# Performance work log

Hardware: AMD Instinct MI355X
Metric: run time of the kernel (lower is better)

The kernel has to match this reference:

```python
import jax, jax.numpy as jnp
from jax import lax
import numpy as np

S, B, D, H, F, K = 1024, 8, 512, 8, 2048, 31
HD = D // H
EPS = 1e-5


def _ln(x, g, b):
    m = jnp.mean(x, axis=-1, keepdims=True)
    v = jnp.mean((x - m) ** 2, axis=-1, keepdims=True)
    return (x - m) * lax.rsqrt(v + EPS) * g + b


def _swish(x):
    return x * jax.nn.sigmoid(x)


def setup_inputs() -> dict:
    key = jax.random.key(0)
    ks = iter(jax.random.split(key, 64))

    def rn(shape, scale=0.02):
        return jax.random.normal(next(ks), shape, dtype=jnp.float32) * scale

    inp = {
        'src': jax.random.normal(next(ks), (S, B, D), dtype=jnp.float32),
        'pos_emb': jax.random.normal(next(ks), (1, 2 * S - 1, D), dtype=jnp.float32),
        # macaron FFN
        'ffm_w1': rn((F, D)), 'ffm_b1': jnp.zeros((F,), jnp.float32),
        'ffm_w2': rn((D, F)), 'ffm_b2': jnp.zeros((D,), jnp.float32),
        # rel-pos MHA
        'in_w': rn((3 * D, D)), 'in_b': jnp.zeros((3 * D,), jnp.float32),
        'out_w': rn((D, D)), 'out_b': jnp.zeros((D,), jnp.float32),
        'pos_w': rn((D, D)),
        'bias_u': rn((H, HD), 0.1), 'bias_v': rn((H, HD), 0.1),
        # conv module
        'pw1_w': rn((2 * D, D)), 'pw1_b': jnp.zeros((2 * D,), jnp.float32),
        'dw_w': rn((D, 1, K)), 'dw_b': jnp.zeros((D,), jnp.float32),
        'cnorm_g': jnp.ones((D,), jnp.float32), 'cnorm_b': jnp.zeros((D,), jnp.float32),
        'pw2_w': rn((D, D)), 'pw2_b': jnp.zeros((D,), jnp.float32),
        # final FFN
        'ff_w1': rn((F, D)), 'ff_b1': jnp.zeros((F,), jnp.float32),
        'ff_w2': rn((D, F)), 'ff_b2': jnp.zeros((D,), jnp.float32),
        # layer norms
        'g_ffm': jnp.ones((D,), jnp.float32), 'b_ffm': jnp.zeros((D,), jnp.float32),
        'g_mha': jnp.ones((D,), jnp.float32), 'b_mha': jnp.zeros((D,), jnp.float32),
        'g_conv': jnp.ones((D,), jnp.float32), 'b_conv': jnp.zeros((D,), jnp.float32),
        'g_ff': jnp.ones((D,), jnp.float32), 'b_ff': jnp.zeros((D,), jnp.float32),
        'g_fin': jnp.ones((D,), jnp.float32), 'b_fin': jnp.zeros((D,), jnp.float32),
    }
    return inp


def _ffn(x, w1, b1, w2, b2):
    return _swish(x @ w1.T + b1) @ w2.T + b2


def _attn(x, pos_emb, in_w, in_b, out_w, out_b, pos_w, bias_u, bias_v):
    # x: (S, B, D)
    qkv = x @ in_w.T + in_b  # (S, B, 3D)
    q, k, v = jnp.split(qkv, 3, axis=-1)
    q = q.reshape(S, B, H, HD).transpose(1, 2, 0, 3)  # (B, H, S, HD)
    k = k.reshape(S, B, H, HD).transpose(1, 2, 0, 3)
    v = v.reshape(S, B, H, HD).transpose(1, 2, 0, 3)
    # positional projection: (2S-1, D) -> (H, HD, 2S-1)
    p = (pos_emb[0] @ pos_w.T).reshape(2 * S - 1, H, HD).transpose(1, 2, 0)
    ac = jnp.einsum('bhsd,bhtd->bhst', q + bias_u[None, :, None, :], k)
    bd = jnp.einsum('bhsd,hdn->bhsn', q + bias_v[None, :, None, :], p)
    # rel_shift: out[b,h,i,j] = bd[b,h,i, (S-1) - i + j]
    idx = (S - 1) - jnp.arange(S)[:, None] + jnp.arange(S)[None, :]  # (S, S)
    bd = jnp.take_along_axis(bd, idx[None, None], axis=-1)  # (B, H, S, S)
    w = jax.nn.softmax((ac + bd) * (HD ** -0.5), axis=-1)
    o = jnp.einsum('bhst,bhtd->bhsd', w, v)
    o = o.transpose(2, 0, 1, 3).reshape(S, B, D)
    return o @ out_w.T + out_b


def _conv_module(x, pw1_w, pw1_b, dw_w, dw_b, cnorm_g, cnorm_b, pw2_w, pw2_b):
    # x: (S, B, D) -> (B, 2D, S)
    y = jnp.einsum('sbd,ed->bes', x, pw1_w) + pw1_b[None, :, None]
    a, g = jnp.split(y, 2, axis=1)
    y = a * jax.nn.sigmoid(g)  # GLU over channels, (B, D, S)
    pad = (K - 1) // 2
    y = lax.conv_general_dilated(y, dw_w, (1,), [(pad, pad)],
                                 dimension_numbers=('NCH', 'OIH', 'NCH'),
                                 feature_group_count=D) + dw_b[None, :, None]
    y = _ln(y.transpose(0, 2, 1), cnorm_g, cnorm_b)  # (B, S, D)
    y = _swish(y)
    y = y @ pw2_w.T + pw2_b  # pointwise conv2 == per-position linear
    return y.transpose(1, 0, 2)  # (S, B, D)


def reference(src, pos_emb, ffm_w1, ffm_b1, ffm_w2, ffm_b2, in_w, in_b, out_w,
              out_b, pos_w, bias_u, bias_v, pw1_w, pw1_b, dw_w, dw_b, cnorm_g,
              cnorm_b, pw2_w, pw2_b, ff_w1, ff_b1, ff_w2, ff_b2, g_ffm, b_ffm,
              g_mha, b_mha, g_conv, b_conv, g_ff, b_ff, g_fin, b_fin):
    x = src
    x = x + 0.5 * _ffn(_ln(x, g_ffm, b_ffm), ffm_w1, ffm_b1, ffm_w2, ffm_b2)
    x = x + _attn(_ln(x, g_mha, b_mha), pos_emb, in_w, in_b, out_w, out_b,
                  pos_w, bias_u, bias_v)
    x = x + _conv_module(_ln(x, g_conv, b_conv), pw1_w, pw1_b, dw_w, dw_b,
                         cnorm_g, cnorm_b, pw2_w, pw2_b)
    x = x + _ffn(_ln(x, g_ff, b_ff), ff_w1, ff_b1, ff_w2, ff_b2)
    return _ln(x, g_fin, b_fin)
```

## Files before the change

### kernel.cpp

```cpp
#include <hip/hip_runtime.h>

typedef __attribute__((ext_vector_type(8))) short bf16x8;
typedef __attribute__((ext_vector_type(4))) short s16x4;
typedef __attribute__((ext_vector_type(4))) float f32x4;
typedef unsigned int u32;

#define SQ 1024
#define BB 8
#define DM 512
#define NH 8
#define HD 64
#define FF 2048
#define NROWS (SQ*BB)

static __device__ __forceinline__ float b2f(short s) {
  return __uint_as_float(((u32)(unsigned short)s) << 16);
}
static __device__ __forceinline__ short f2b(float f) {
  u32 u = __float_as_uint(f);
  return (short)((u + 0x7FFFu + ((u >> 16) & 1u)) >> 16);
}
static __device__ __forceinline__ short f2bt(float f) {
  return (short)((__float_as_uint(f) + 0x8000u) >> 16);
}
static __device__ __forceinline__ float sigm(float x) { return 1.f / (1.f + __expf(-x)); }

static __device__ __forceinline__ f32x4 mfma16(bf16x8 a, bf16x8 b, f32x4 c) {
  return __builtin_amdgcn_mfma_f32_16x16x32_bf16(a, b, c, 0, 0, 0);
}

static __device__ __forceinline__ void gload16(const void* g, void* l) {
  __builtin_amdgcn_global_load_lds(
      (const __attribute__((address_space(1))) void*)g,
      (__attribute__((address_space(3))) void*)l, 16, 0, 0);
}

static __device__ __forceinline__ int swzp(int r, int byteoff) {
  return (r * 128 + byteoff) ^ ((r & 7) << 4);
}

#define WAIT_LGKM() do { \
    asm volatile("s_waitcnt lgkmcnt(0)" ::: "memory"); \
    __builtin_amdgcn_sched_barrier(0); } while (0)
#define WAIT_VM(n) do { \
    asm volatile("s_waitcnt vmcnt(" #n ")" ::: "memory"); \
    __builtin_amdgcn_sched_barrier(0); } while (0)

struct CvtArgs {
  const float* s[10];
  short* d[10];
  int n4[10];
  int cum[10];
};
__global__ __launch_bounds__(256) void cvt_multi(CvtArgs a) {
  int bid = blockIdx.x;
  int seg = 0;
#pragma unroll
  for (int i = 1; i < 10; ++i) if (bid >= a.cum[i]) seg = i;
  int idx = (bid - a.cum[seg]) * 256 + threadIdx.x;
  if (idx >= a.n4[seg]) return;
  float4 v = ((const float4*)a.s[seg])[idx];
  s16x4 r = { f2b(v.x), f2b(v.y), f2b(v.z), f2b(v.w) };
  ((s16x4*)a.d[seg])[idx] = r;
}

template<int MODE, int INF32>
__global__ __launch_bounds__(256) void ln_kernel(const void* __restrict__ xin,
                                                 const float* __restrict__ gam,
                                                 const float* __restrict__ bet,
                                                 void* __restrict__ out) {
  int w = threadIdx.x >> 6, lane = threadIdx.x & 63;
  int row = (blockIdx.x << 2) + w;
  float v[8];
  if (INF32) {
    const float* xr = (const float*)xin + (size_t)row * DM + lane * 8;
    float4 a = *(const float4*)xr;
    float4 c = *(const float4*)(xr + 4);
    v[0]=a.x; v[1]=a.y; v[2]=a.z; v[3]=a.w; v[4]=c.x; v[5]=c.y; v[6]=c.z; v[7]=c.w;
  } else {
    bf16x8 x8 = *(const bf16x8*)((const short*)xin + (size_t)row * DM + lane * 8);
#pragma unroll
    for (int e = 0; e < 8; ++e) v[e] = b2f(x8[e]);
  }
  float s = 0.f, q = 0.f;
#pragma unroll
  for (int e = 0; e < 8; ++e) { s += v[e]; q += v[e] * v[e]; }
#pragma unroll
  for (int m = 1; m < 64; m <<= 1) { s += __shfl_xor(s, m); q += __shfl_xor(q, m); }
  float mean = s * (1.f / DM);
  float rstd = rsqrtf(q * (1.f / DM) - mean * mean + 1e-5f);
  int col = lane * 8;
  if (MODE == 1) {
    float* o = (float*)out + (size_t)row * DM + col;
    float y[8];
#pragma unroll
    for (int e = 0; e < 8; ++e) y[e] = (v[e] - mean) * rstd * gam[col + e] + bet[col + e];
    *(float4*)o = make_float4(y[0], y[1], y[2], y[3]);
    *(float4*)(o + 4) = make_float4(y[4], y[5], y[6], y[7]);
  } else {
    bf16x8 r;
#pragma unroll
    for (int e = 0; e < 8; ++e) {
      float y = (v[e] - mean) * rstd * gam[col + e] + bet[col + e];
      r[e] = f2b(y);
    }
    *(bf16x8*)((short*)out + (size_t)row * DM + col) = r;
  }
}

template<int EPI>
__global__ __launch_bounds__(512, 2) void gemm256(const short* __restrict__ A,
                                                  const short* __restrict__ W,
                                                  const float* __restrict__ bias,
                                                  short* __restrict__ out,
                                                  int M, int N, int K) {
  __shared__ __align__(16) short lds[3 * 16384];
  int nb = N >> 8;
  int nwg = gridDim.x, bid = blockIdx.x;
  int bid2 = ((nwg & 7) == 0) ? ((bid & 7) * (nwg >> 3) + (bid >> 3)) : bid;
  int bm = bid2 / nb, bn = bid2 % nb;
  int m0 = bm << 8, n0 = bn << 8;
  int tid = threadIdx.x, w = tid >> 6, lane = tid & 63;
  int wm = w >> 2, wn = w & 3;
  int l15 = lane & 15, l4 = lane >> 4;
  int srow = lane >> 2;
  int slog = (lane & 3) ^ (((lane >> 5) & 1) << 1);
  int scol = slog << 3;

  const short* gsrc = (w < 4) ? (A + (size_t)(m0 + w * 64 + srow) * K + scol)
                              : (W + (size_t)(n0 + (w - 4) * 64 + srow) * K + scol);

  f32x4 acc[8][4];
#pragma unroll
  for (int i = 0; i < 8; ++i)
#pragma unroll
    for (int j = 0; j < 4; ++j) acc[i][j] = (f32x4){0.f, 0.f, 0.f, 0.f};

  auto stage2 = [&](int u, int kt, int q0) {
#pragma unroll
    for (int q = q0; q < q0 + 2; ++q)
      gload16(gsrc + (size_t)(q * 16) * K + kt,
              (char*)lds + u * 32768 + (w * 4 + q) * 1024);
  };
  auto rdA = [&](int u, int mf) -> bf16x8 {
    int ps = l4 ^ (((l15 >> 3) & 1) << 1);
    return *(const bf16x8*)((char*)lds + u * 32768 + (wm * 8 + mf) * 1024 + l15 * 64 + ps * 16);
  };
  auto rdB = [&](int u, int nf) -> bf16x8 {
    int ps = l4 ^ (((l15 >> 3) & 1) << 1);
    return *(const bf16x8*)((char*)lds + u * 32768 + 16384 + (wn * 4 + nf) * 1024 + l15 * 64 + ps * 16);
  };

  int nt = K >> 5;
  stage2(0, 0, 0); stage2(0, 0, 2);
  stage2(1, 32, 0); stage2(1, 32, 2);
  WAIT_VM(4);
  __builtin_amdgcn_s_barrier();

  int u = 0;
  for (int t = 0; t < nt; ++t) {
    int kt2 = (t + 2) << 5;
    int us = u + 2; if (us >= 3) us -= 3;
    bool st = (t + 2) < nt;
    bf16x8 afrag[4], bfrag[4];
#pragma unroll
    for (int nf = 0; nf < 4; ++nf) bfrag[nf] = rdB(u, nf);
#pragma unroll
    for (int mf = 0; mf < 4; ++mf) afrag[mf] = rdA(u, mf);
    if (st) stage2(us, kt2, 0);
    __builtin_amdgcn_s_barrier();
    WAIT_LGKM();
    __builtin_amdgcn_s_setprio(1);
#pragma unroll
    for (int mf = 0; mf < 4; ++mf)
#pragma unroll
      for (int nf = 0; nf < 4; ++nf)
        acc[mf][nf] = mfma16(afrag[mf], bfrag[nf], acc[mf][nf]);
    __builtin_amdgcn_s_setprio(0);
    __builtin_amdgcn_s_barrier();
#pragma unroll
    for (int mf = 0; mf < 4; ++mf) afrag[mf] = rdA(u, mf + 4);
    if (st) stage2(us, kt2, 2);
    __builtin_amdgcn_s_barrier();
    WAIT_LGKM();
    __builtin_amdgcn_s_setprio(1);
#pragma unroll
    for (int mf = 0; mf < 4; ++mf)
#pragma unroll
      for (int nf = 0; nf < 4; ++nf)
        acc[mf + 4][nf] = mfma16(afrag[mf], bfrag[nf], acc[mf + 4][nf]);
    __builtin_amdgcn_s_setprio(0);
    if (t < nt - 1) {
      if (st) { WAIT_VM(4); } else { WAIT_VM(0); }
    }
    __builtin_amdgcn_s_barrier();
    ++u; if (u >= 3) u -= 3;
  }

#pragma unroll
  for (int nf = 0; nf < 4; ++nf) {
    int col = n0 + wn * 64 + nf * 16 + l15;
    float bv = bias[col];
#pragma unroll
    for (int mf = 0; mf < 8; ++mf) {
#pragma unroll
      for (int r4 = 0; r4 < 4; ++r4) {
        int row = m0 + wm * 128 + mf * 16 + l4 * 4 + r4;
        float v = acc[mf][nf][r4] + bv;
        if (EPI == 1) v = v * sigm(v);
        out[(size_t)row * N + col] = f2b(v);
      }
    }
  }
}

template<int EPI, int RESF32>
__global__ __launch_bounds__(256, 3) void gemm128(const short* __restrict__ A,
                                                  const short* __restrict__ W,
                                                  const float* __restrict__ bias,
                                                  const void* __restrict__ res,
                                                  float alpha, short* __restrict__ out,
                                                  int M, int N, int K) {
  __shared__ __align__(16) short lds[3 * 8192];
  int nb = N >> 7;
  int nwg = gridDim.x, bid = blockIdx.x;
  int bid2 = ((nwg & 7) == 0) ? ((bid & 7) * (nwg >> 3) + (bid >> 3)) : bid;
  int bm = bid2 / nb, bn = bid2 % nb;
  int m0 = bm << 7, n0 = bn << 7;
  int tid = threadIdx.x, w = tid >> 6, lane = tid & 63;
  int wm = w >> 1, wn = w & 1;
  int l15 = lane & 15, l4 = lane >> 4;
  int srow = lane >> 2;
  int slog = (lane & 3) ^ (((lane >> 5) & 1) << 1);
  int scol = slog << 3;

  const short* gsrc = (w < 2) ? (A + (size_t)(m0 + w * 64 + srow) * K + scol)
                              : (W + (size_t)(n0 + (w - 2) * 64 + srow) * K + scol);
  int ldsbase = w * 4096;

  f32x4 acc[4][4];
#pragma unroll
  for (int i = 0; i < 4; ++i)
#pragma unroll
    for (int j = 0; j < 4; ++j) acc[i][j] = (f32x4){0.f, 0.f, 0.f, 0.f};

  auto stage = [&](int u, int kt) {
#pragma unroll
    for (int q = 0; q < 4; ++q)
      gload16(gsrc + (size_t)(q * 16) * K + kt,
              (char*)lds + u * 16384 + ldsbase + q * 1024);
  };
  auto rdA = [&](int u, int mf) -> bf16x8 {
    int ps = l4 ^ (((l15 >> 3) & 1) << 1);
    return *(const bf16x8*)((char*)lds + u * 16384 + (wm * 4 + mf) * 1024 + l15 * 64 + ps * 16);
  };
  auto rdB = [&](int u, int nf) -> bf16x8 {
    int ps = l4 ^ (((l15 >> 3) & 1) << 1);
    return *(const bf16x8*)((char*)lds + u * 16384 + 8192 + (wn * 4 + nf) * 1024 + l15 * 64 + ps * 16);
  };

  int nt = K >> 5;
  stage(0, 0);
  stage(1, 32);
  WAIT_VM(4);
  __builtin_amdgcn_s_barrier();

  int u = 0;
  for (int t = 0; t < nt; ++t) {
    int us = u + 2; if (us >= 3) us -= 3;
    bool st = (t + 2) < nt;
    bf16x8 afrag[4], bfrag[4];
#pragma unroll
    for (int mf = 0; mf < 4; ++mf) afrag[mf] = rdA(u, mf);
#pragma unroll
    for (int nf = 0; nf < 4; ++nf) bfrag[nf] = rdB(u, nf);
    if (st) stage(us, (t + 2) << 5);
    WAIT_LGKM();
    __builtin_amdgcn_s_setprio(1);
#pragma unroll
    for (int mf = 0; mf < 4; ++mf)
#pragma unroll
      for (int nf = 0; nf < 4; ++nf)
        acc[mf][nf] = mfma16(afrag[mf], bfrag[nf], acc[mf][nf]);
    __builtin_amdgcn_s_setprio(0);
    if (t < nt - 1) {
      if (st) { WAIT_VM(4); } else { WAIT_VM(0); }
    }
    __builtin_amdgcn_s_barrier();
    ++u; if (u >= 3) u -= 3;
  }

#pragma unroll
  for (int mf = 0; mf < 4; ++mf) {
#pragma unroll
    for (int nf = 0; nf < 4; ++nf) {
      int col = n0 + wn * 64 + nf * 16 + l15;
      float bv = (EPI == 3) ? 0.f : bias[col];
#pragma unroll
      for (int r4 = 0; r4 < 4; ++r4) {
        int row = m0 + wm * 64 + mf * 16 + l4 * 4 + r4;
        size_t idx = (size_t)row * N + col;
        float v = acc[mf][nf][r4] + bv;
        if (EPI == 0 || EPI == 3) {
          out[idx] = f2b(v);
        } else if (EPI == 1) {
          out[idx] = f2b(v * sigm(v));
        } else {
          float rv = RESF32 ? ((const float*)res)[idx] : b2f(((const short*)res)[idx]);
          out[idx] = f2b(rv + alpha * v);
        }
      }
    }
  }
}

__global__ __launch_bounds__(256) void prep_kernel(const short* __restrict__ qkv,
                                                   short* __restrict__ VTp) {
  __shared__ short ldsv[64 * 66];
  int tid = threadIdx.x;
  int st = blockIdx.x & 15, bh = blockIdx.x >> 4;
  int b = bh >> 3, h = bh & 7;
  int s0 = st << 6;
#pragma unroll
  for (int pass = 0; pass < 2; ++pass) {
    int r = pass * 32 + (tid >> 3), c = tid & 7;
    int s = s0 + r;
    bf16x8 v8 = *(const bf16x8*)(qkv + (size_t)(s * BB + b) * 1536 + 1024 + h * 64 + c * 8);
    *(bf16x8*)(ldsv + r * 66 + c * 8) = v8;
  }
  __syncthreads();
#pragma unroll
  for (int pass = 0; pass < 2; ++pass) {
    int d = pass * 32 + (tid >> 3), sc = tid & 7;
    bf16x8 o;
#pragma unroll
    for (int u = 0; u < 8; ++u) o[u] = ldsv[(sc * 8 + u) * 66 + d];
    *(bf16x8*)(VTp + ((size_t)bh * 64 + d) * SQ + s0 + sc * 8) = o;
  }
}

__global__ __launch_bounds__(512, 4) void attn_kernel(const short* __restrict__ qkv,
                                                      const short* __restrict__ VTp,
                                                      const short* __restrict__ posb,
                                                      const float* __restrict__ bias_u,
                                                      const float* __restrict__ bias_v,
                                                      short* __restrict__ obuf) {
  __shared__ __align__(16) char smem[78848];
  char* lds_k   = smem;
  char* lds_vt  = smem + 16384;
  char* lds_pos = smem + 24576;
  char* lds_ew  = smem + 57344;

  int tid = threadIdx.x, w = tid >> 6, lane = tid & 63;
  int l15 = lane & 15, l4 = lane >> 4;
  int it = blockIdx.x >> 6, bh = blockIdx.x & 63;
  int b = bh >> 3, h = bh & 7;
  int i0 = it << 7;
  char* ewb = lds_ew + w * 2688;

  const size_t hoffB = (size_t)bh * SQ * 128;

  const float SC2 = 0.125f * 1.44269504f;
  int fr = i0 + w * 16 + l15;
  const short* qrow = qkv + (size_t)(fr * BB + b) * 1536 + h * 64;
  bf16x8 qu_f[2], qv_f[2];
#pragma unroll
  for (int ks = 0; ks < 2; ++ks) {
    bf16x8 qraw = *(const bf16x8*)(qrow + ks * 32 + l4 * 8);
#pragma unroll
    for (int e = 0; e < 8; ++e) {
      float qf = b2f(qraw[e]);
      int d = h * 64 + ks * 32 + l4 * 8 + e;
      qu_f[ks][e] = f2b((qf + bias_u[d]) * SC2);
      qv_f[ks][e] = f2b((qf + bias_v[d]) * SC2);
    }
  }

  float m_run = -1e30f, l_run = 0.f;
  f32x4 o_acc[4];
#pragma unroll
  for (int dt = 0; dt < 4; ++dt) o_acc[dt] = (f32x4){0.f, 0.f, 0.f, 0.f};

  int prbase = 112 - 16 * w;
  int lnq = lane >> 3, lnr = lane & 7;
  int r8 = w * 8 + lnq;
  int byt = (lnr * 16) ^ ((r8 & 7) << 4);
  int nbase = 896 - i0;

  auto stageK = [&](int t1) {
    int j = (t1 << 6) + r8;
    gload16((const char*)qkv + (size_t)(j * BB + b) * 3072 + 1024 + h * 128 + byt,
            lds_k + (t1 & 1) * 8192 + w * 1024);
  };
  auto stageVT = [&](int t1) {
    gload16((const char*)VTp + hoffB + (size_t)r8 * 2048 + (size_t)(t1 << 7) + byt,
            lds_vt + w * 1024);
  };
  auto stagePosSeg = [&](int gbase, int pseg) {
    gload16((const char*)posb + (size_t)(gbase + r8) * 1024 + h * 128 + byt,
            lds_pos + pseg * 8192 + w * 1024);
  };

  stagePosSeg(nbase, 0);
  stagePosSeg(nbase + 64, 1);
  stagePosSeg(nbase + 128, 2);
  stageK(0);
  WAIT_VM(0);

  for (int t = 0; t < 16; ++t) {
    int cur = t & 1;
    __builtin_amdgcn_s_barrier();
    stageVT(t);

    f32x4 acs[4];
    __builtin_amdgcn_s_setprio(1);
#pragma unroll
    for (int kt = 0; kt < 4; ++kt) {
      f32x4 z = (f32x4){0.f, 0.f, 0.f, 0.f};
      bf16x8 kb0 = *(const bf16x8*)(lds_k + cur * 8192 + swzp(kt * 16 + l15, l4 * 16));
      bf16x8 kb1 = *(const bf16x8*)(lds_k + cur * 8192 + swzp(kt * 16 + l15, 64 + l4 * 16));
      z = mfma16(kb0, qu_f[0], z);
      z = mfma16(kb1, qu_f[1], z);
      acs[kt] = z;
    }
    __builtin_amdgcn_s_setprio(0);
#pragma unroll
    for (int pt = 0; pt < 5; ++pt) {
      f32x4 z = (f32x4){0.f, 0.f, 0.f, 0.f};
      int pr = prbase + pt * 16 + l15;
      char* pbase = lds_pos + (((t + (pr >> 6)) & 3) * 8192);
      bf16x8 pb0 = *(const bf16x8*)(pbase + swzp(pr & 63, l4 * 16));
      bf16x8 pb1 = *(const bf16x8*)(pbase + swzp(pr & 63, 64 + l4 * 16));
      __builtin_amdgcn_s_setprio(1);
      z = mfma16(pb0, qv_f[0], z);
      z = mfma16(pb1, qv_f[1], z);
      __builtin_amdgcn_s_setprio(0);
      s16x4 ek;
#pragma unroll
      for (int r = 0; r < 4; ++r) ek[r] = f2bt(z[r]);
      *(s16x4*)(ewb + (l15 * 84 + pt * 16 + l4 * 4) * 2) = ek;
    }

    bool pf = (t + 1) < 16;
    if (pf) {
      stageK(t + 1);
      stagePosSeg(nbase + (t << 6) + 192, (t + 3) & 3);
    }

    WAIT_LGKM();

    float sv[4][4];
#pragma unroll
    for (int kt = 0; kt < 4; ++kt) {
#pragma unroll
      for (int r = 0; r < 4; ++r) {
        int n = 15 - l15 + kt * 16 + l4 * 4 + r;
        float ev = b2f(*(const short*)(ewb + (l15 * 84 + n) * 2));
        sv[kt][r] = acs[kt][r] + ev;
      }
    }
    float mk[4];
#pragma unroll
    for (int kt = 0; kt < 4; ++kt)
      mk[kt] = fmaxf(fmaxf(sv[kt][0], sv[kt][1]), fmaxf(sv[kt][2], sv[kt][3]));
    float mt = fmaxf(fmaxf(mk[0], mk[1]), fmaxf(mk[2], mk[3]));

    if (!__all(mt <= m_run + 11.5415604f)) {
      float mr = fmaxf(mt, __shfl_xor(mt, 16));
      mr = fmaxf(mr, __shfl_xor(mr, 32));
      float mn = fmaxf(m_run, mr);
      float fac = exp2f(m_run - mn);
      m_run = mn;
      l_run *= fac;
      float fb[4];
#pragma unroll
      for (int r4 = 0; r4 < 4; ++r4) fb[r4] = __shfl(fac, (l4 << 2) + r4);
#pragma unroll
      for (int dt = 0; dt < 4; ++dt)
#pragma unroll
        for (int r4 = 0; r4 < 4; ++r4) o_acc[dt][r4] *= fb[r4];
    }
    float lsk[4];
#pragma unroll
    for (int kt = 0; kt < 4; ++kt) {
      s16x4 pk;
      float p[4];
#pragma unroll
      for (int r = 0; r < 4; ++r) {
        p[r] = exp2f(sv[kt][r] - m_run);
        pk[r] = f2bt(p[r]);
      }
      lsk[kt] = (p[0] + p[1]) + (p[2] + p[3]);
      *(s16x4*)(ewb + l15 * 128 + ((kt * 32 + l4 * 8) ^ ((l15 & 7) << 4))) = pk;
    }
    l_run += (lsk[0] + lsk[1]) + (lsk[2] + lsk[3]);

    if (pf) { WAIT_VM(2); } else { WAIT_VM(0); }
    WAIT_LGKM();
    __builtin_amdgcn_s_barrier();

    bf16x8 pa[2];
#pragma unroll
    for (int ks = 0; ks < 2; ++ks)
      pa[ks] = *(const bf16x8*)(ewb + swzp(l15, ks * 64 + l4 * 16));
    __builtin_amdgcn_s_setprio(1);
#pragma unroll
    for (int dt = 0; dt < 4; ++dt) {
      bf16x8 vb0 = *(const bf16x8*)(lds_vt + swzp(dt * 16 + l15, l4 * 16));
      bf16x8 vb1 = *(const bf16x8*)(lds_vt + swzp(dt * 16 + l15, 64 + l4 * 16));
      o_acc[dt] = mfma16(pa[0], vb0, o_acc[dt]);
      o_acc[dt] = mfma16(pa[1], vb1, o_acc[dt]);
    }
    __builtin_amdgcn_s_setprio(0);

    WAIT_VM(0);
  }

  float lt = l_run + __shfl_xor(l_run, 16);
  lt += __shfl_xor(lt, 32);
  float lb[4];
#pragma unroll
  for (int r4 = 0; r4 < 4; ++r4) lb[r4] = __shfl(lt, (l4 << 2) + r4);
#pragma unroll
  for (int dt = 0; dt < 4; ++dt) {
#pragma unroll
    for (int r4 = 0; r4 < 4; ++r4) {
      int i = i0 + w * 16 + l4 * 4 + r4;
      int d = dt * 16 + l15;
      float val = o_acc[dt][r4] / lb[r4];
      obuf[(size_t)(i * BB + b) * DM + h * 64 + d] = f2b(val);
    }
  }
}

__global__ __launch_bounds__(256) void glu_dwconv_kernel(const short* __restrict__ pw1,
                                                         const float* __restrict__ dww,
                                                         const float* __restrict__ dwb,
                                                         const float* __restrict__ cg,
                                                         const float* __restrict__ cb,
                                                         short* __restrict__ outbf) {
  __shared__ short glu[38 * 512];
  __shared__ float red[8][4][2];
  int tid = threadIdx.x;
  int b = blockIdx.x & 7;
  int s0 = (blockIdx.x >> 3) << 3;
  for (int idx = tid; idx < 38 * 64; idx += 256) {
    int r = idx >> 6, c8 = idx & 63;
    int s = s0 - 15 + r;
    bf16x8 res;
    if (s >= 0 && s < SQ) {
      const short* row = pw1 + (size_t)(s * BB + b) * 1024;
      bf16x8 a8 = *(const bf16x8*)(row + c8 * 8);
      bf16x8 g8 = *(const bf16x8*)(row + 512 + c8 * 8);
#pragma unroll
      for (int e = 0; e < 8; ++e) res[e] = f2b(b2f(a8[e]) * sigm(b2f(g8[e])));
    } else {
#pragma unroll
      for (int e = 0; e < 8; ++e) res[e] = 0;
    }
    *(bf16x8*)(glu + r * 512 + c8 * 8) = res;
  }
  __syncthreads();

  float a0[8], a1[8];
  {
    float wreg[31];
#pragma unroll
    for (int k = 0; k < 31; ++k) wreg[k] = dww[tid * 31 + k];
    float bb = dwb[tid];
    for (int ri = 0; ri < 8; ++ri) {
      float acc = bb;
#pragma unroll
      for (int k = 0; k < 31; ++k)
        acc += wreg[k] * b2f(glu[(ri + k) * 512 + tid]);
      a0[ri] = acc;
    }
  }
  {
    int d = tid + 256;
    float wreg[31];
#pragma unroll
    for (int k = 0; k < 31; ++k) wreg[k] = dww[d * 31 + k];
    float bb = dwb[d];
    for (int ri = 0; ri < 8; ++ri) {
      float acc = bb;
#pragma unroll
      for (int k = 0; k < 31; ++k)
        acc += wreg[k] * b2f(glu[(ri + k) * 512 + d]);
      a1[ri] = acc;
    }
  }

  int w = tid >> 6, lane = tid & 63;
#pragma unroll
  for (int ri = 0; ri < 8; ++ri) {
    float sp = a0[ri] + a1[ri];
    float qp = a0[ri] * a0[ri] + a1[ri] * a1[ri];
#pragma unroll
    for (int m = 1; m < 64; m <<= 1) { sp += __shfl_xor(sp, m); qp += __shfl_xor(qp, m); }
    if (lane == 0) { red[ri][w][0] = sp; red[ri][w][1] = qp; }
  }
  __syncthreads();
  float g0 = cg[tid], b0 = cb[tid], g1 = cg[tid + 256], b1 = cb[tid + 256];
#pragma unroll
  for (int ri = 0; ri < 8; ++ri) {
    float s = red[ri][0][0] + red[ri][1][0] + red[ri][2][0] + red[ri][3][0];
    float q = red[ri][0][1] + red[ri][1][1] + red[ri][2][1] + red[ri][3][1];
    float mean = s * (1.f / DM);
    float rstd = rsqrtf(q * (1.f / DM) - mean * mean + 1e-5f);
    float y0 = (a0[ri] - mean) * rstd * g0 + b0;
    float y1 = (a1[ri] - mean) * rstd * g1 + b1;
    y0 = y0 * sigm(y0);
    y1 = y1 * sigm(y1);
    size_t base = (size_t)((s0 + ri) * BB + b) * 512;
    outbf[base + tid] = f2b(y0);
    outbf[base + tid + 256] = f2b(y1);
  }
}

extern "C" void kernel_launch(void* const* d_in, const int* in_sizes, int n_in,
                              void* d_out, int out_size, void* d_ws, size_t ws_size,
                              hipStream_t stream) {
  const float* src    = (const float*)d_in[0];
  const float* pose   = (const float*)d_in[1];
  const float* ffm_w1 = (const float*)d_in[2];
  const float* ffm_b1 = (const float*)d_in[3];
  const float* ffm_w2 = (const float*)d_in[4];
  const float* ffm_b2 = (const float*)d_in[5];
  const float* in_w   = (const float*)d_in[6];
  const float* in_b   = (const float*)d_in[7];
  const float* out_w  = (const float*)d_in[8];
  const float* out_b  = (const float*)d_in[9];
  const float* pos_w  = (const float*)d_in[10];
  const float* bias_u = (const float*)d_in[11];
  const float* bias_v = (const float*)d_in[12];
  const float* pw1_w  = (const float*)d_in[13];
  const float* pw1_b  = (const float*)d_in[14];
  const float* dw_w   = (const float*)d_in[15];
  const float* dw_b   = (const float*)d_in[16];
  const float* cng    = (const float*)d_in[17];
  const float* cnb    = (const float*)d_in[18];
  const float* pw2_w  = (const float*)d_in[19];
  const float* pw2_b  = (const float*)d_in[20];
  const float* ff_w1  = (const float*)d_in[21];
  const float* ff_b1  = (const float*)d_in[22];
  const float* ff_w2  = (const float*)d_in[23];
  const float* ff_b2  = (const float*)d_in[24];
  const float* g_ffm  = (const float*)d_in[25];
  const float* b_ffm  = (const float*)d_in[26];
  const float* g_mha  = (const float*)d_in[27];
  const float* b_mha  = (const float*)d_in[28];
  const float* g_conv = (const float*)d_in[29];
  const float* b_conv = (const float*)d_in[30];
  const float* g_ff   = (const float*)d_in[31];
  const float* b_ff   = (const float*)d_in[32];
  const float* g_fin  = (const float*)d_in[33];
  const float* b_fin  = (const float*)d_in[34];

  char* ws = (char*)d_ws;
  size_t off = 0;
  auto alloc = [&](size_t bytes) -> void* {
    void* p = ws + off;
    off += (bytes + 255) & ~(size_t)255;
    return p;
  };
  short* wb_ffm1 = (short*)alloc((size_t)FF * DM * 2);
  short* wb_ffm2 = (short*)alloc((size_t)DM * FF * 2);
  short* wb_in   = (short*)alloc((size_t)3 * DM * DM * 2);
  short* wb_out  = (short*)alloc((size_t)DM * DM * 2);
  short* wb_pos  = (short*)alloc((size_t)DM * DM * 2);
  short* wb_pw1  = (short*)alloc((size_t)2 * DM * DM * 2);
  short* wb_pw2  = (short*)alloc((size_t)DM * DM * 2);
  short* wb_ff1  = (short*)alloc((size_t)FF * DM * 2);
  short* wb_ff2  = (short*)alloc((size_t)DM * FF * 2);
  short* pos_src = (short*)alloc((size_t)2048 * DM * 2);
  short* pos_bf  = (short*)alloc((size_t)2048 * DM * 2);
  short* lnb     = (short*)alloc((size_t)NROWS * DM * 2);
  short* hbig    = (short*)alloc((size_t)NROWS * FF * 2);
  short* qkvb    = (short*)alloc((size_t)NROWS * 3 * DM * 2);
  short* obuf    = (short*)alloc((size_t)NROWS * DM * 2);
  short* x1      = (short*)alloc((size_t)NROWS * DM * 2);
  short* x2      = (short*)alloc((size_t)NROWS * DM * 2);
  short* pw1raw  = hbig;
  short* convy   = obuf;
  short* x3 = x1;
  short* x4 = x2;
  short* VTp = hbig + (size_t)3 * 4194304;

  CvtArgs ca;
  const float* srcs[10] = {ffm_w1, ffm_w2, in_w, out_w, pos_w, pw1_w, pw2_w, ff_w1, ff_w2, pose};
  short* dsts[10] = {wb_ffm1, wb_ffm2, wb_in, wb_out, wb_pos, wb_pw1, wb_pw2, wb_ff1, wb_ff2, pos_src};
  size_t ns[10] = {(size_t)FF*DM, (size_t)DM*FF, (size_t)3*DM*DM, (size_t)DM*DM, (size_t)DM*DM,
                   (size_t)2*DM*DM, (size_t)DM*DM, (size_t)FF*DM, (size_t)DM*FF, (size_t)2047*DM};
  int cum = 0;
  for (int i = 0; i < 10; ++i) {
    ca.s[i] = srcs[i]; ca.d[i] = dsts[i];
    ca.n4[i] = (int)(ns[i] >> 2);
    ca.cum[i] = cum;
    cum += (ca.n4[i] + 255) / 256;
  }
  cvt_multi<<<dim3(cum), dim3(256), 0, stream>>>(ca);

  auto gemmR = [&](int RESF32, const short* A, const short* W, const float* bias,
                   const void* res, float alpha, short* out, int M, int N, int K) {
    dim3 g((M / 128) * (N / 128)), blk(256);
    if (RESF32) gemm128<2, 1><<<g, blk, 0, stream>>>(A, W, bias, res, alpha, out, M, N, K);
    else        gemm128<2, 0><<<g, blk, 0, stream>>>(A, W, bias, res, alpha, out, M, N, K);
  };
  auto gemm2 = [&](int EPI, const short* A, const short* W, const float* bias,
                   short* out, int M, int N, int K) {
    dim3 g((M / 256) * (N / 256)), blk(512);
    if (EPI == 0) gemm256<0><<<g, blk, 0, stream>>>(A, W, bias, out, M, N, K);
    else          gemm256<1><<<g, blk, 0, stream>>>(A, W, bias, out, M, N, K);
  };

  gemm128<3, 0><<<dim3((2048 / 128) * (512 / 128)), dim3(256), 0, stream>>>(
      pos_src, wb_pos, nullptr, nullptr, 0.f, pos_bf, 2048, DM, DM);

  ln_kernel<0, 1><<<dim3(NROWS / 4), dim3(256), 0, stream>>>(src, g_ffm, b_ffm, lnb);
  gemm2(1, lnb, wb_ffm1, ffm_b1, hbig, NROWS, FF, DM);
  gemmR(1, hbig, wb_ffm2, ffm_b2, src, 0.5f, x1, NROWS, DM, FF);

  ln_kernel<0, 0><<<dim3(NROWS / 4), dim3(256), 0, stream>>>(x1, g_mha, b_mha, lnb);
  gemm128<0, 0><<<dim3((NROWS / 128) * (3 * DM / 128)), dim3(256), 0, stream>>>(
      lnb, wb_in, in_b, nullptr, 0.f, qkvb, NROWS, 3 * DM, DM);
  prep_kernel<<<dim3(1024), dim3(256), 0, stream>>>(qkvb, VTp);
  attn_kernel<<<dim3(512), dim3(512), 0, stream>>>(qkvb, VTp, pos_bf, bias_u, bias_v, obuf);
  gemmR(0, obuf, wb_out, out_b, x1, 1.f, x2, NROWS, DM, DM);

  ln_kernel<0, 0><<<dim3(NROWS / 4), dim3(256), 0, stream>>>(x2, g_conv, b_conv, lnb);
  gemm128<0, 0><<<dim3((NROWS / 128) * (2 * DM / 128)), dim3(256), 0, stream>>>(
      lnb, wb_pw1, pw1_b, nullptr, 0.f, pw1raw, NROWS, 2 * DM, DM);
  glu_dwconv_kernel<<<dim3(1024), dim3(256), 0, stream>>>(pw1raw, dw_w, dw_b, cng, cnb, convy);
  gemmR(0, convy, wb_pw2, pw2_b, x2, 1.f, x3, NROWS, DM, DM);

  ln_kernel<0, 0><<<dim3(NROWS / 4), dim3(256), 0, stream>>>(x3, g_ff, b_ff, lnb);
  gemm2(1, lnb, wb_ff1, ff_b1, hbig, NROWS, FF, DM);
  gemmR(0, hbig, wb_ff2, ff_b2, x3, 1.f, x4, NROWS, DM, FF);

  ln_kernel<1, 0><<<dim3(NROWS / 4), dim3(256), 0, stream>>>(x4, g_fin, b_fin, d_out);

  (void)in_sizes; (void)n_in; (void)out_size; (void)ws_size;
}
```

Baseline: 321.9 us.

## Use split-K with fp32 partial sums for FFN down-projection GEMMs

```diff
diff --git a/kernel.cpp b/kernel.cpp
--- a/kernel.cpp
+++ b/kernel.cpp
@@ -312,6 +312,121 @@
       }
     }
   }
+}
+
+__global__ __launch_bounds__(256, 3) void gemm128sk(const short* __restrict__ A,
+                                                    const short* __restrict__ W,
+                                                    float* __restrict__ psum,
+                                                    int M, int N, int K) {
+  __shared__ __align__(16) short lds[3 * 8192];
+  int nb = N >> 7;
+  int nwg_t = gridDim.x >> 1;
+  int half = (blockIdx.x >= nwg_t) ? 1 : 0;
+  int bid = blockIdx.x - half * nwg_t;
+  int bid2 = ((nwg_t & 7) == 0) ? ((bid & 7) * (nwg_t >> 3) + (bid >> 3)) : bid;
+  int bm = bid2 / nb, bn = bid2 % nb;
+  int m0 = bm << 7, n0 = bn << 7;
+  int kbase = half * (K >> 1);
+  int tid = threadIdx.x, w = tid >> 6, lane = tid & 63;
+  int wm = w >> 1, wn = w & 1;
+  int l15 = lane & 15, l4 = lane >> 4;
+  int srow = lane >> 2;
+  int slog = (lane & 3) ^ (((lane >> 5) & 1) << 1);
+  int scol = slog << 3;
+
+  const short* gsrc = (w < 2) ? (A + (size_t)(m0 + w * 64 + srow) * K + kbase + scol)
+                              : (W + (size_t)(n0 + (w - 2) * 64 + srow) * K + kbase + scol);
+  int ldsbase = w * 4096;
+
+  f32x4 acc[4][4];
+#pragma unroll
+  for (int i = 0; i < 4; ++i)
+#pragma unroll
+    for (int j = 0; j < 4; ++j) acc[i][j] = (f32x4){0.f, 0.f, 0.f, 0.f};
+
+  auto stage = [&](int u, int kt) {
+#pragma unroll
+    for (int q = 0; q < 4; ++q)
+      gload16(gsrc + (size_t)(q * 16) * K + kt,
+              (char*)lds + u * 16384 + ldsbase + q * 1024);
+  };
+  auto rdA = [&](int u, int mf) -> bf16x8 {
+    int ps = l4 ^ (((l15 >> 3) & 1) << 1);
+    return *(const bf16x8*)((char*)lds + u * 16384 + (wm * 4 + mf) * 1024 + l15 * 64 + ps * 16);
+  };
+  auto rdB = [&](int u, int nf) -> bf16x8 {
+    int ps = l4 ^ (((l15 >> 3) & 1) << 1);
+    return *(const bf16x8*)((char*)lds + u * 16384 + 8192 + (wn * 4 + nf) * 1024 + l15 * 64 + ps * 16);
+  };
+
+  int nt = K >> 6;
+  stage(0, 0);
+  stage(1, 32);
+  WAIT_VM(4);
+  __builtin_amdgcn_s_barrier();
+
+  int u = 0;
+  for (int t = 0; t < nt; ++t) {
+    int us = u + 2; if (us >= 3) us -= 3;
+    bool st = (t + 2) < nt;
+    bf16x8 afrag[4], bfrag[4];
+#pragma unroll
+    for (int mf = 0; mf < 4; ++mf) afrag[mf] = rdA(u, mf);
+#pragma unroll
+    for (int nf = 0; nf < 4; ++nf) bfrag[nf] = rdB(u, nf);
+    if (st) stage(us, (t + 2) << 5);
+    WAIT_LGKM();
+    __builtin_amdgcn_s_setprio(1);
+#pragma unroll
+    for (int mf = 0; mf < 4; ++mf)
+#pragma unroll
+      for (int nf = 0; nf < 4; ++nf)
+        acc[mf][nf] = mfma16(afrag[mf], bfrag[nf], acc[mf][nf]);
+    __builtin_amdgcn_s_setprio(0);
+    if (t < nt - 1) {
+      if (st) { WAIT_VM(4); } else { WAIT_VM(0); }
+    }
+    __builtin_amdgcn_s_barrier();
+    ++u; if (u >= 3) u -= 3;
+  }
+
+  float* dst = psum + (size_t)half * M * N;
+#pragma unroll
+  for (int mf = 0; mf < 4; ++mf) {
+#pragma unroll
+    for (int nf = 0; nf < 4; ++nf) {
+      int col = n0 + wn * 64 + nf * 16 + l15;
+#pragma unroll
+      for (int r4 = 0; r4 < 4; ++r4) {
+        int row = m0 + wm * 64 + mf * 16 + l4 * 4 + r4;
+        dst[(size_t)row * N + col] = acc[mf][nf][r4];
+      }
+    }
+  }
+}
+
+template<int RESF32>
+__global__ __launch_bounds__(256) void combine_sk(const float* __restrict__ psum,
+                                                  const float* __restrict__ bias,
+                                                  const void* __restrict__ res,
+                                                  float alpha, short* __restrict__ out,
+                                                  int M, int N) {
+  int idx4 = blockIdx.x * 256 + threadIdx.x;
+  if (idx4 >= (M * N) >> 2) return;
+  size_t off = (size_t)idx4 << 2;
+  f32x4 p0 = *(const f32x4*)(psum + off);
+  f32x4 p1 = *(const f32x4*)(psum + (size_t)M * N + off);
+  int col0 = (int)(off & (size_t)(N - 1));
+  s16x4 r;
+#pragma unroll
+  for (int e = 0; e < 4; ++e) {
+    float v = p0[e] + p1[e] + bias[col0 + e];
+    float rv;
+    if (RESF32) rv = ((const float*)res)[off + e];
+    else        rv = b2f(((const short*)res)[off + e]);
+    r[e] = f2b(rv + alpha * v);
+  }
+  *(s16x4*)(out + off) = r;
 }
 
 __global__ __launch_bounds__(256) void prep_kernel(const short* __restrict__ qkv,
@@ -681,6 +796,7 @@
   short* obuf    = (short*)alloc((size_t)NROWS * DM * 2);
   short* x1      = (short*)alloc((size_t)NROWS * DM * 2);
   short* x2      = (short*)alloc((size_t)NROWS * DM * 2);
+  float* psum    = (float*)alloc((size_t)2 * NROWS * DM * 4);
   short* pw1raw  = hbig;
   short* convy   = obuf;
   short* x3 = x1;
@@ -707,6 +823,14 @@
     if (RESF32) gemm128<2, 1><<<g, blk, 0, stream>>>(A, W, bias, res, alpha, out, M, N, K);
     else        gemm128<2, 0><<<g, blk, 0, stream>>>(A, W, bias, res, alpha, out, M, N, K);
   };
+  auto gemmRsk = [&](int RESF32, const short* A, const short* W, const float* bias,
+                     const void* res, float alpha, short* out, int M, int N, int K) {
+    dim3 g(2 * (M / 128) * (N / 128)), blk(256);
+    gemm128sk<<<g, blk, 0, stream>>>(A, W, psum, M, N, K);
+    dim3 gc((M * N / 4 + 255) / 256);
+    if (RESF32) combine_sk<1><<<gc, dim3(256), 0, stream>>>(psum, bias, res, alpha, out, M, N);
+    else        combine_sk<0><<<gc, dim3(256), 0, stream>>>(psum, bias, res, alpha, out, M, N);
+  };
   auto gemm2 = [&](int EPI, const short* A, const short* W, const float* bias,
                    short* out, int M, int N, int K) {
     dim3 g((M / 256) * (N / 256)), blk(512);
@@ -719,7 +843,7 @@
 
   ln_kernel<0, 1><<<dim3(NROWS / 4), dim3(256), 0, stream>>>(src, g_ffm, b_ffm, lnb);
   gemm2(1, lnb, wb_ffm1, ffm_b1, hbig, NROWS, FF, DM);
-  gemmR(1, hbig, wb_ffm2, ffm_b2, src, 0.5f, x1, NROWS, DM, FF);
+  gemmRsk(1, hbig, wb_ffm2, ffm_b2, src, 0.5f, x1, NROWS, DM, FF);
 
   ln_kernel<0, 0><<<dim3(NROWS / 4), dim3(256), 0, stream>>>(x1, g_mha, b_mha, lnb);
   gemm128<0, 0><<<dim3((NROWS / 128) * (3 * DM / 128)), dim3(256), 0, stream>>>(
@@ -736,7 +860,7 @@
 
   ln_kernel<0, 0><<<dim3(NROWS / 4), dim3(256), 0, stream>>>(x3, g_ff, b_ff, lnb);
   gemm2(1, lnb, wb_ff1, ff_b1, hbig, NROWS, FF, DM);
-  gemmR(0, hbig, wb_ff2, ff_b2, x3, 1.f, x4, NROWS, DM, FF);
+  gemmRsk(0, hbig, wb_ff2, ff_b2, x3, 1.f, x4, NROWS, DM, FF);
 
   ln_kernel<1, 0><<<dim3(NROWS / 4), dim3(256), 0, stream>>>(x4, g_fin, b_fin, d_out);
 
```

After: 337.9 us. 5.0% more time.
